# Performance work log

Hardware: AMD Instinct MI355X
Metric: run time of the kernel (lower is better)

The kernel has to match this reference:

```python
import jax, jax.numpy as jnp
import numpy as np
from jax import lax

B, H_IMG, W_IMG, DIM, HEADS = 8, 128, 128, 192, 8
SPLIT = (4, 16)
HB = HEADS // 2            # heads per branch
CB = DIM // 2              # channels per branch
POS_DIM = (CB // 4) // 4   # DynamicPosBias hidden dim = 6


def _make_rel(Hsp, Wsp):
    # rpe_biases table coords and relative_position_index, exactly as in torch buffers
    bh = np.arange(1 - Hsp, Hsp)
    bw = np.arange(1 - Wsp, Wsp)
    biases = np.stack(np.meshgrid(bh, bw, indexing='ij')).reshape(2, -1).T.astype(np.float32)
    coords = np.stack(np.meshgrid(np.arange(Hsp), np.arange(Wsp), indexing='ij')).reshape(2, -1)
    rel = (coords[:, :, None] - coords[:, None, :]).transpose(1, 2, 0).copy()
    rel[:, :, 0] += Hsp - 1
    rel[:, :, 1] += Wsp - 1
    rel[:, :, 0] *= 2 * Wsp - 1
    return jnp.asarray(biases), jnp.asarray(rel.sum(-1))


def _ln(x, g, b):
    m = x.mean(-1, keepdims=True)
    v = ((x - m) ** 2).mean(-1, keepdims=True)
    return (x - m) * lax.rsqrt(v + 1e-5) * g + b


def _dyn_bias(bi, pw, pb, g1, b1, w1, c1, g2, b2, w2, c2, g3, b3, w3, c3):
    # residual=False path: pos3(pos2(pos1(pos_proj(biases)))); posN = Linear(ReLU(LN(.)))
    p = bi @ pw.T + pb
    p = jax.nn.relu(_ln(p, g1, b1)) @ w1.T + c1
    p = jax.nn.relu(_ln(p, g2, b2)) @ w2.T + c2
    return jax.nn.relu(_ln(p, g3, b3)) @ w3.T + c3  # (M, HB)


def _branch(q, k, v, H, W, Hsp, Wsp, rel_idx, biases, pp):
    Bq, L, Cb = q.shape
    N = Hsp * Wsp
    hd = Cb // HB
    def win(t):  # (B, L, Cb) -> (B*nW, HB, N, hd)
        t = t.reshape(Bq, H // Hsp, Hsp, W // Wsp, Wsp, Cb).transpose(0, 1, 3, 2, 4, 5)
        return t.reshape(-1, N, HB, hd).transpose(0, 2, 1, 3)
    qw, kw, vw = win(q), win(k), win(v)
    attn = jnp.einsum('whnd,whmd->whnm', qw * (hd ** -0.5), kw)
    pos = _dyn_bias(biases, *pp)
    rpb = pos[rel_idx.reshape(-1)].reshape(N, N, HB).transpose(2, 0, 1)  # (HB, N, N)
    attn = jax.nn.softmax(attn + rpb[None], axis=-1)
    z = jnp.einsum('whnm,whmd->whnd', attn, vw).transpose(0, 2, 1, 3).reshape(-1, N, Cb)
    z = z.reshape(Bq, H // Hsp, W // Wsp, Hsp, Wsp, Cb).transpose(0, 1, 3, 2, 4, 5)
    return z.reshape(Bq, H * W, Cb)


def _bn(x, g, b, m, v):  # eval-mode BatchNorm2d, NCHW
    sc = (g * lax.rsqrt(v + 1e-5))[None, :, None, None]
    return (x - m[None, :, None, None]) * sc + b[None, :, None, None]


def _fwd(x1, x2, qkv_w, proj_w, proj_b, pw, pb, g1, b1, w1, c1, g2, b2, w2, c2,
         g3, b3, w3, c3, dw_w, dw_b, bn1_g, bn1_b, bn1_m, bn1_v,
         si_w1, si_b1, bn2_g, bn2_b, bn2_m, bn2_v, si_w2, si_b2, H, W):
    Bx, L, C = x1.shape
    qkv1 = (x1 @ qkv_w.T).reshape(Bx, L, 3, C)
    qkv2 = (x2 @ qkv_w.T).reshape(Bx, L, 3, C)
    q1, v1 = qkv1[:, :, 0], qkv1[:, :, 2]
    k2 = qkv2[:, :, 1]
    Ch = C // 2
    bi0, ri0 = _make_rel(SPLIT[0], SPLIT[1])  # idx=0: Hsp, Wsp = split
    bi1, ri1 = _make_rel(SPLIT[1], SPLIT[0])  # idx=1: swapped
    pos_all = (pw, pb, g1, b1, w1, c1, g2, b2, w2, c2, g3, b3, w3, c3)
    pp0 = tuple(a[0] for a in pos_all)
    pp1 = tuple(a[1] for a in pos_all)
    xa = _branch(q1[..., :Ch], k2[..., :Ch], v1[..., :Ch], H, W, SPLIT[0], SPLIT[1], ri0, bi0, pp0)
    xb = _branch(q1[..., Ch:], k2[..., Ch:], v1[..., Ch:], H, W, SPLIT[1], SPLIT[0], ri1, bi1, pp1)
    attened = jnp.concatenate([xa, xb], axis=-1)  # (B, L, C)
    # conv branch: depthwise 3x3 + BN + GELU on v
    v_img = v1.transpose(0, 2, 1).reshape(Bx, C, H, W)
    conv_x = lax.conv_general_dilated(v_img, dw_w, (1, 1), 'SAME',
                                      feature_group_count=C,
                                      dimension_numbers=('NCHW', 'OIHW', 'NCHW'))
    conv_x = conv_x + dw_b[None, :, None, None]
    conv_x = jax.nn.gelu(_bn(conv_x, bn1_g, bn1_b, bn1_m, bn1_v), approximate=False)
    # spatial interaction map from the attention branch (1x1 conv -> BN -> GELU -> 1x1 conv)
    attn_img = attened.transpose(0, 2, 1).reshape(Bx, C, H, W)
    s = jnp.einsum('oc,bchw->bohw', si_w1, attn_img) + si_b1[None, :, None, None]
    s = jax.nn.gelu(_bn(s, bn2_g, bn2_b, bn2_m, bn2_v), approximate=False)
    s = jnp.einsum('oc,bchw->bohw', si_w2, s) + si_b2[None, :, None, None]  # (B,1,H,W)
    conv_x = jax.nn.sigmoid(s) * conv_x
    conv_x = conv_x.transpose(0, 2, 3, 1).reshape(Bx, L, C)
    return (attened + conv_x) @ proj_w.T + proj_b


def setup_inputs() -> dict:
    key = jax.random.key(0)
    ks = jax.random.split(key, 16)
    L = H_IMG * W_IMG
    def n(k, shape, s=0.05):
        return jax.random.normal(k, shape, jnp.float32) * s
    d = {}
    d['x1'] = jax.random.normal(ks[0], (B, L, DIM), jnp.float32)
    d['x2'] = jax.random.normal(ks[1], (B, L, DIM), jnp.float32)
    d['qkv_w'] = n(ks[2], (3 * DIM, DIM))
    d['proj_w'] = n(ks[3], (DIM, DIM))
    d['proj_b'] = jnp.zeros((DIM,), jnp.float32)
    d['pw'] = n(ks[4], (2, POS_DIM, 2), 0.2)
    d['pb'] = jnp.zeros((2, POS_DIM), jnp.float32)
    d['g1'] = jnp.ones((2, POS_DIM), jnp.float32); d['b1'] = jnp.zeros((2, POS_DIM), jnp.float32)
    d['w1'] = n(ks[5], (2, POS_DIM, POS_DIM), 0.2); d['c1'] = jnp.zeros((2, POS_DIM), jnp.float32)
    d['g2'] = jnp.ones((2, POS_DIM), jnp.float32); d['b2'] = jnp.zeros((2, POS_DIM), jnp.float32)
    d['w2'] = n(ks[6], (2, POS_DIM, POS_DIM), 0.2); d['c2'] = jnp.zeros((2, POS_DIM), jnp.float32)
    d['g3'] = jnp.ones((2, POS_DIM), jnp.float32); d['b3'] = jnp.zeros((2, POS_DIM), jnp.float32)
    d['w3'] = n(ks[7], (2, HB, POS_DIM), 0.2); d['c3'] = jnp.zeros((2, HB), jnp.float32)
    d['dw_w'] = n(ks[8], (DIM, 1, 3, 3), 0.2); d['dw_b'] = jnp.zeros((DIM,), jnp.float32)
    d['bn1_g'] = jnp.ones((DIM,), jnp.float32); d['bn1_b'] = jnp.zeros((DIM,), jnp.float32)
    d['bn1_m'] = n(ks[9], (DIM,), 0.1)
    d['bn1_v'] = jax.random.uniform(ks[10], (DIM,), jnp.float32, 0.5, 1.5)
    d['si_w1'] = n(ks[11], (DIM // 2, DIM)); d['si_b1'] = jnp.zeros((DIM // 2,), jnp.float32)
    d['bn2_g'] = jnp.ones((DIM // 2,), jnp.float32); d['bn2_b'] = jnp.zeros((DIM // 2,), jnp.float32)
    d['bn2_m'] = n(ks[12], (DIM // 2,), 0.1)
    d['bn2_v'] = jax.random.uniform(ks[13], (DIM // 2,), jnp.float32, 0.5, 1.5)
    d['si_w2'] = n(ks[14], (1, DIM // 2), 0.2); d['si_b2'] = jnp.zeros((1,), jnp.float32)
    d['H'] = H_IMG
    d['W'] = W_IMG
    return d


def reference(x1, x2, qkv_w, proj_w, proj_b, pw, pb, g1, b1, w1, c1, g2, b2, w2, c2,
              g3, b3, w3, c3, dw_w, dw_b, bn1_g, bn1_b, bn1_m, bn1_v,
              si_w1, si_b1, bn2_g, bn2_b, bn2_m, bn2_v, si_w2, si_b2, H, W):
    return _fwd(x1, x2, qkv_w, proj_w, proj_b, pw, pb, g1, b1, w1, c1, g2, b2, w2, c2,
                g3, b3, w3, c3, dw_w, dw_b, bn1_g, bn1_b, bn1_m, bn1_v,
                si_w1, si_b1, bn2_g, bn2_b, bn2_m, bn2_v, si_w2, si_b2, int(H), int(W))
```

## Files before the change

### kernel.cpp

```cpp
#include <hip/hip_runtime.h>
#include <hip/hip_bf16.h>
#include <math.h>

#define BDIM 8
#define HH 128
#define WW 128
#define LL (HH*WW)
#define CC 192
#define CBh 96
#define HBn 4
#define HDd 24
#define PD 6
#define RTAB 217

typedef unsigned short ushortT;
typedef __bf16 bf16x8 __attribute__((ext_vector_type(8)));
typedef float f32x4 __attribute__((ext_vector_type(4)));

__device__ __forceinline__ float b2f(ushortT u){
  union { float f; unsigned u; } x; x.u = ((unsigned)u) << 16; return x.f;
}
__device__ __forceinline__ ushortT f2b(float f){
  union { float f; unsigned u; } x; x.f = f;
  unsigned r = x.u + 0x7fffu + ((x.u >> 16) & 1u);
  return (ushortT)(r >> 16);
}
__device__ __forceinline__ float lo16(unsigned u){ union { float f; unsigned u; } x; x.u = u << 16; return x.f; }
__device__ __forceinline__ float hi16(unsigned u){ union { float f; unsigned u; } x; x.u = u & 0xffff0000u; return x.f; }
__device__ __forceinline__ unsigned pack2(float a, float b){
  return (unsigned)f2b(a) | ((unsigned)f2b(b) << 16);
}
__device__ __forceinline__ void unpack8(uint4 u, float* f){
  f[0]=lo16(u.x); f[1]=hi16(u.x); f[2]=lo16(u.y); f[3]=hi16(u.y);
  f[4]=lo16(u.z); f[5]=hi16(u.z); f[6]=lo16(u.w); f[7]=hi16(u.w);
}
__device__ __forceinline__ unsigned cvt2(float a, float b){
  __hip_bfloat162 h = __float22bfloat162_rn(float2{a, b});
  union { __hip_bfloat162 h; unsigned u; } c; c.h = h; return c.u;
}
__device__ __forceinline__ float gelu_exact(float x){
  return 0.5f * x * (1.0f + erff(x * 0.70710678118654752f));
}

union ABu { unsigned u[4]; bf16x8 v; };

__device__ __forceinline__ void stage_B512(const ushortT* __restrict__ Wsrc, char* lds){
  int t = threadIdx.x;
  #pragma unroll
  for (int i = 0; i < 9; i++){
    int c = t + i*512;
    int n = c / 24, kc = c - n*24;
    uint4 v = *(const uint4*)(const void*)(Wsrc + n*CC + kc*8);
    int byte = n*384 + kc*16;
    byte ^= ((n & 7) << 4);
    *(uint4*)(lds + byte) = v;
  }
}
__device__ __forceinline__ bf16x8 ldsB(const char* lds, int row, int kbyte){
  int byte = row*384 + kbyte;
  byte ^= ((row & 7) << 4);
  return *(const bf16x8*)(lds + byte);
}

__device__ __forceinline__ void ln_relu6(float* p, const float* g, const float* b){
  float m = 0.f;
  #pragma unroll
  for (int j=0;j<PD;j++) m += p[j];
  m *= (1.0f/PD);
  float v = 0.f;
  #pragma unroll
  for (int j=0;j<PD;j++){ float d = p[j]-m; v += d*d; }
  v *= (1.0f/PD);
  float is = rsqrtf(v + 1e-5f);
  #pragma unroll
  for (int j=0;j<PD;j++){ float t = (p[j]-m)*is*g[j] + b[j]; p[j] = t > 0.f ? t : 0.f; }
}
__device__ __forceinline__ void mm6(float* p, const float* w, const float* c){
  float q[PD];
  #pragma unroll
  for (int j=0;j<PD;j++){
    float a = c[j];
    #pragma unroll
    for (int i=0;i<PD;i++) a += p[i]*w[j*PD+i];
    q[j] = a;
  }
  #pragma unroll
  for (int j=0;j<PD;j++) p[j] = q[j];
}

__global__ void k_pos(const float* __restrict__ pw, const float* __restrict__ pb,
                      const float* __restrict__ g1, const float* __restrict__ b1,
                      const float* __restrict__ w1, const float* __restrict__ c1,
                      const float* __restrict__ g2, const float* __restrict__ b2,
                      const float* __restrict__ w2, const float* __restrict__ c2,
                      const float* __restrict__ g3, const float* __restrict__ b3,
                      const float* __restrict__ w3, const float* __restrict__ c3,
                      float* __restrict__ pos){
  int br = blockIdx.x;
  int r = threadIdx.x;
  if (r >= RTAB) return;
  int Hsp = br ? 16 : 4, Wsp = br ? 4 : 16;
  int W2 = 2*Wsp - 1;
  float bi0 = (float)(r / W2 - (Hsp-1));
  float bi1 = (float)(r % W2 - (Wsp-1));
  const float* PW = pw + br*PD*2;
  const float* PB = pb + br*PD;
  float p[PD];
  #pragma unroll
  for (int j=0;j<PD;j++) p[j] = PW[j*2]*bi0 + PW[j*2+1]*bi1 + PB[j];
  ln_relu6(p, g1+br*PD, b1+br*PD);
  mm6(p, w1+br*PD*PD, c1+br*PD);
  ln_relu6(p, g2+br*PD, b2+br*PD);
  mm6(p, w2+br*PD*PD, c2+br*PD);
  ln_relu6(p, g3+br*PD, b3+br*PD);
  const float* W3 = w3 + br*HBn*PD;
  const float* C3 = c3 + br*HBn;
  #pragma unroll
  for (int h=0;h<HBn;h++){
    float a = C3[h];
    #pragma unroll
    for (int i=0;i<PD;i++) a += p[i]*W3[h*PD+i];
    pos[((size_t)br*RTAB + r)*HBn + h] = a;
  }
}

#define WQKV_ELEMS (3*CC*CC)
#define WPROJ_ELEMS (CC*CC)
#define WSI_ELEMS (CC*CBh)
#define WALL_PAIRS ((WQKV_ELEMS+WPROJ_ELEMS+WSI_ELEMS)/2)

__global__ void k_cvtw(const float* __restrict__ qkv_w, const float* __restrict__ proj_w,
                       const float* __restrict__ si_w1,
                       const float* __restrict__ si_b1,
                       const float* __restrict__ g, const float* __restrict__ bb,
                       const float* __restrict__ mn, const float* __restrict__ vv,
                       const float* __restrict__ si_w2,
                       const float* __restrict__ dw_w, const float* __restrict__ dw_b,
                       const float* __restrict__ bn1_g, const float* __restrict__ bn1_b,
                       const float* __restrict__ bn1_m, const float* __restrict__ bn1_v,
                       ushortT* __restrict__ wb, float* __restrict__ gparam,
                       float* __restrict__ cparam, ushortT* __restrict__ dwt){
  int t = threadIdx.x;
  if (blockIdx.x == 0 && t < CBh){
    float sc = g[t]*rsqrtf(vv[t]+1e-5f);
    gparam[t]        = sc;
    gparam[CBh+t]    = (si_b1[t]-mn[t])*sc + bb[t];
    gparam[2*CBh+t]  = si_w2[t];
  }
  if (blockIdx.x == 1){
    if (t < CC){
      float sc = bn1_g[t]*rsqrtf(bn1_v[t]+1e-5f);
      cparam[t]      = sc;
      cparam[CC+t]   = (dw_b[t]-bn1_m[t])*sc + bn1_b[t];
    }
    for (int i = t; i < 9*CC; i += 256){
      int k = i / CC, c = i - k*CC;
      dwt[i] = f2b(dw_w[c*9 + k]);
    }
  }
  int i = blockIdx.x*256 + t;
  if (i >= WALL_PAIRS) return;
  int e = i*2;
  float a, b;
  if (e < WQKV_ELEMS){ a = qkv_w[e]; b = qkv_w[e+1]; }
  else if (e < WQKV_ELEMS+WPROJ_ELEMS){ a = proj_w[e-WQKV_ELEMS]; b = proj_w[e-WQKV_ELEMS+1]; }
  else { a = si_w1[e-WQKV_ELEMS-WPROJ_ELEMS]; b = si_w1[e-WQKV_ELEMS-WPROJ_ELEMS+1]; }
  *(unsigned*)(void*)(wb + e) = cvt2(a, b);
}

__global__ __launch_bounds__(512, 4) void k_qkv(const float* __restrict__ x1, const float* __restrict__ x2,
                                                const ushortT* __restrict__ wb,
                                                ushortT* __restrict__ q1, ushortT* __restrict__ k2,
                                                ushortT* __restrict__ v1){
  __shared__ char Bs[CC*CC*2];
  int z = blockIdx.y;
  const float* src = (z == 1) ? x2 : x1;
  ushortT* dst = (z == 0) ? q1 : ((z == 1) ? k2 : v1);
  stage_B512(wb + (size_t)z*CC*CC, Bs);

  int w = threadIdx.x >> 6, l = threadIdx.x & 63;
  int row0 = blockIdx.x*128 + w*16;
  int lr = l & 15;
  int hk = l >> 4;
  f32x4 acc[12];
  #pragma unroll
  for (int n=0; n<12; n++) acc[n] = (f32x4){0.f,0.f,0.f,0.f};

  const float* ap = src + (size_t)(row0 + lr)*CC + hk*8;
  __syncthreads();

  #pragma unroll
  for (int ks = 0; ks < 6; ks++){
    float4 p0 = *(const float4*)(ap + ks*32);
    float4 p1 = *(const float4*)(ap + ks*32 + 4);
    ABu a;
    a.u[0] = cvt2(p0.x, p0.y); a.u[1] = cvt2(p0.z, p0.w);
    a.u[2] = cvt2(p1.x, p1.y); a.u[3] = cvt2(p1.z, p1.w);
    int kb = ks*64 + hk*16;
    #pragma unroll
    for (int n=0; n<12; n++){
      bf16x8 bfr = ldsB(Bs, n*16 + lr, kb);
      acc[n] = __builtin_amdgcn_mfma_f32_16x16x32_bf16(a.v, bfr, acc[n], 0, 0, 0);
    }
  }
  int crow = hk*4, ccol = lr;
  #pragma unroll
  for (int n=0; n<12; n++)
    #pragma unroll
    for (int r=0; r<4; r++){
      int m = row0 + crow + r;
      dst[(size_t)m*CC + n*16 + ccol] = f2b(acc[n][r]);
    }
}

template<int HSP, int WSP>
__global__ __launch_bounds__(256) void k_attn(const ushortT* __restrict__ q1, const ushortT* __restrict__ k2,
                                              const ushortT* __restrict__ v1, const float* __restrict__ pos,
                                              ushortT* __restrict__ att){
  constexpr int BR = (HSP == 4) ? 0 : 1;
  constexpr int NWH = HH / HSP, NWW = WW / WSP;
  constexpr int CH0 = BR * CBh;
  __shared__ float ks[64][CBh];
  __shared__ float vs[64][CBh];
  __shared__ float ps[RTAB*HBn];
  int t = threadIdx.x;
  int wid = blockIdx.x;
  int b = wid / (NWH*NWW);
  int rem = wid - b*(NWH*NWW);
  int hi = rem / NWW, wj = rem - hi*NWW;
  for (int i = t; i < RTAB*HBn; i += 256) ps[i] = pos[(size_t)BR*RTAB*HBn + i];
  #pragma unroll
  for (int r = 0; r < 3; r++){
    int idx = t + r*256;
    int pix = idx / 12, seg = idx - pix*12;
    int ii = pix / WSP, jj = pix - ii*WSP;
    size_t base = (((size_t)b*LL) + (size_t)(hi*HSP+ii)*WW + wj*WSP + jj)*CC + CH0 + seg*8;
    uint4 uk = *(const uint4*)(const void*)(k2 + base);
    unpack8(uk, &ks[pix][seg*8]);
    uint4 uv = *(const uint4*)(const void*)(v1 + base);
    unpack8(uv, &vs[pix][seg*8]);
  }
  __syncthreads();
  int h = t >> 6, lane = t & 63;
  int i1 = lane / WSP, j1 = lane - i1*WSP;
  size_t lq = ((size_t)b*LL) + (size_t)(hi*HSP+i1)*WW + wj*WSP + j1;
  const ushortT* qrow = q1 + lq*CC + CH0 + h*HDd;
  float qf[HDd];
  #pragma unroll
  for (int d0 = 0; d0 < HDd; d0 += 8){
    uint4 u = *(const uint4*)(const void*)(qrow + d0);
    unpack8(u, &qf[d0]);
  }
  #pragma unroll
  for (int d=0; d<HDd; d++) qf[d] *= 0.20412414523193154f;
  float lg[64];
  #pragma unroll
  for (int m = 0; m < 64; m++){
    const float* kr = &ks[m][h*HDd];
    float s = 0.f;
    #pragma unroll
    for (int d=0; d<HDd; d++) s = fmaf(qf[d], kr[d], s);
    int i2 = m / WSP, j2 = m - i2*WSP;
    int ridx = (i1-i2+HSP-1)*(2*WSP-1) + (j1-j2+WSP-1);
    lg[m] = s + ps[ridx*HBn + h];
  }
  float mx = lg[0];
  #pragma unroll
  for (int m=1;m<64;m++) mx = fmaxf(mx, lg[m]);
  float sum = 0.f;
  #pragma unroll
  for (int m=0;m<64;m++){ lg[m] = __expf(lg[m]-mx); sum += lg[m]; }
  float inv = 1.0f / sum;
  float z[HDd];
  #pragma unroll
  for (int d=0;d<HDd;d++) z[d] = 0.f;
  #pragma unroll
  for (int m=0;m<64;m++){
    float p = lg[m]*inv;
    const float* vr = &vs[m][h*HDd];
    #pragma unroll
    for (int d=0;d<HDd;d++) z[d] = fmaf(p, vr[d], z[d]);
  }
  ushortT* orow = att + lq*CC + CH0 + h*HDd;
  #pragma unroll
  for (int d0=0; d0<HDd; d0+=8){
    uint4 u;
    u.x = pack2(z[d0+0], z[d0+1]);
    u.y = pack2(z[d0+2], z[d0+3]);
    u.z = pack2(z[d0+4], z[d0+5]);
    u.w = pack2(z[d0+6], z[d0+7]);
    *(uint4*)(void*)(orow + d0) = u;
  }
}

__global__ __launch_bounds__(256) void k_conv(const ushortT* __restrict__ v1,
                                              const ushortT* __restrict__ dwt,
                                              const float* __restrict__ cparam,
                                              ushortT* __restrict__ cx){
  int tid = blockIdx.x*256 + threadIdx.x;
  int grp = tid % 24;
  int pix = tid / 24;
  int j = pix & (WW-1);
  int rest = pix >> 7;
  int i = rest & (HH-1);
  int b = rest >> 7;
  int c0 = grp*8;
  uint4 wreg[9];
  #pragma unroll
  for (int k=0;k<9;k++) wreg[k] = *(const uint4*)(const void*)(dwt + k*CC + c0);
  float acc[8];
  #pragma unroll
  for (int t2=0;t2<8;t2++) acc[t2]=0.f;
  #pragma unroll
  for (int ki=0;ki<3;ki++){
    int ii = i + ki - 1;
    if (ii < 0 || ii >= HH) continue;
    #pragma unroll
    for (int kj=0;kj<3;kj++){
      int jj = j + kj - 1;
      if (jj < 0 || jj >= WW) continue;
      uint4 uv = *(const uint4*)(const void*)(v1 + (((size_t)b*LL) + (size_t)ii*WW + jj)*CC + c0);
      float fv[8], fw[8];
      unpack8(uv, fv);
      unpack8(wreg[ki*3+kj], fw);
      #pragma unroll
      for (int t2=0;t2<8;t2++) acc[t2] = fmaf(fv[t2], fw[t2], acc[t2]);
    }
  }
  float4 s0 = *(const float4*)(cparam + c0);
  float4 s1 = *(const float4*)(cparam + c0 + 4);
  float4 o0 = *(const float4*)(cparam + CC + c0);
  float4 o1 = *(const float4*)(cparam + CC + c0 + 4);
  float scv[8] = {s0.x,s0.y,s0.z,s0.w,s1.x,s1.y,s1.z,s1.w};
  float ofv[8] = {o0.x,o0.y,o0.z,o0.w,o1.x,o1.y,o1.z,o1.w};
  unsigned ou[4];
  #pragma unroll
  for (int t2=0;t2<4;t2++){
    float y0 = gelu_exact(acc[2*t2]  *scv[2*t2]   + ofv[2*t2]);
    float y1 = gelu_exact(acc[2*t2+1]*scv[2*t2+1] + ofv[2*t2+1]);
    ou[t2] = pack2(y0, y1);
  }
  uint4 res; res.x=ou[0]; res.y=ou[1]; res.z=ou[2]; res.w=ou[3];
  *(uint4*)(void*)(cx + (size_t)pix*CC + c0) = res;
}

__global__ __launch_bounds__(256) void k_gate(const ushortT* __restrict__ att,
                                              const ushortT* __restrict__ wsi,
                                              const float* __restrict__ gparam,
                                              const float* __restrict__ si_b2,
                                              float* __restrict__ gate){
  int w = threadIdx.x >> 6, l = threadIdx.x & 63;
  int row0 = blockIdx.x*128 + w*32;
  int lr = l & 15;
  int lk = (l >> 4) * 8;
  f32x4 acc[2][6];
  #pragma unroll
  for (int rt=0; rt<2; rt++)
    #pragma unroll
    for (int n=0; n<6; n++) acc[rt][n] = (f32x4){0.f,0.f,0.f,0.f};
  #pragma unroll
  for (int ks = 0; ks < 6; ks++){
    int k0 = ks*32 + lk;
    bf16x8 a0 = *(const bf16x8*)(const void*)(att + (size_t)(row0 + lr)*CC + k0);
    bf16x8 a1 = *(const bf16x8*)(const void*)(att + (size_t)(row0 + 16 + lr)*CC + k0);
    #pragma unroll
    for (int n=0; n<6; n++){
      bf16x8 bfr = *(const bf16x8*)(const void*)(wsi + (size_t)(n*16 + lr)*CC + k0);
      acc[0][n] = __builtin_amdgcn_mfma_f32_16x16x32_bf16(a0, bfr, acc[0][n], 0, 0, 0);
      acc[1][n] = __builtin_amdgcn_mfma_f32_16x16x32_bf16(a1, bfr, acc[1][n], 0, 0, 0);
    }
  }
  int crow = (l >> 4) * 4, ccol = l & 15;
  float sc6[6], cb6[6], w26[6];
  #pragma unroll
  for (int n=0; n<6; n++){
    int o = n*16 + ccol;
    sc6[n] = gparam[o];
    cb6[n] = gparam[CBh + o];
    w26[n] = gparam[2*CBh + o];
  }
  float sb2 = si_b2[0];
  float ps[2][4];
  #pragma unroll
  for (int rt=0; rt<2; rt++)
    #pragma unroll
    for (int r=0; r<4; r++) ps[rt][r] = 0.f;
  #pragma unroll
  for (int rt=0; rt<2; rt++)
    #pragma unroll
    for (int n=0; n<6; n++)
      #pragma unroll
      for (int r=0; r<4; r++){
        float x = acc[rt][n][r]*sc6[n] + cb6[n];
        ps[rt][r] += gelu_exact(x) * w26[n];
      }
  #pragma unroll
  for (int rt=0; rt<2; rt++)
    #pragma unroll
    for (int r=0; r<4; r++){
      float v = ps[rt][r];
      #pragma unroll
      for (int off = 1; off < 16; off <<= 1) v += __shfl_xor(v, off, 64);
      ps[rt][r] = v;
    }
  if (ccol == 0){
    #pragma unroll
    for (int rt=0; rt<2; rt++)
      #pragma unroll
      for (int r=0; r<4; r++){
        int m = row0 + rt*16 + crow + r;
        gate[m] = 1.0f / (1.0f + __expf(-(ps[rt][r] + sb2)));
      }
  }
}

__global__ __launch_bounds__(512, 4) void k_proj(const ushortT* __restrict__ att, const ushortT* __restrict__ cx,
                                                 const float* __restrict__ gate,
                                                 const ushortT* __restrict__ wp, const float* __restrict__ pbias,
                                                 float* __restrict__ out){
  __shared__ char Bs[CC*CC*2];
  stage_B512(wp, Bs);

  int w = threadIdx.x >> 6, l = threadIdx.x & 63;
  int row0 = blockIdx.x*128 + w*16;
  int lr = l & 15;
  int hk = l >> 4;
  float gv = gate[row0 + lr];
  f32x4 acc[12];
  #pragma unroll
  for (int n=0; n<12; n++) acc[n] = (f32x4){0.f,0.f,0.f,0.f};

  size_t base = (size_t)(row0 + lr)*CC + hk*8;
  __syncthreads();

  #pragma unroll
  for (int ks = 0; ks < 6; ks++){
    uint4 ua = *(const uint4*)(const void*)(att + base + ks*32);
    uint4 uc = *(const uint4*)(const void*)(cx  + base + ks*32);
    float fa[8], fc[8];
    unpack8(ua, fa); unpack8(uc, fc);
    #pragma unroll
    for (int j=0;j<8;j++) fa[j] = fmaf(gv, fc[j], fa[j]);
    ABu a;
    a.u[0] = cvt2(fa[0], fa[1]); a.u[1] = cvt2(fa[2], fa[3]);
    a.u[2] = cvt2(fa[4], fa[5]); a.u[3] = cvt2(fa[6], fa[7]);
    int kb = ks*64 + hk*16;
    #pragma unroll
    for (int n=0; n<12; n++){
      bf16x8 bfr = ldsB(Bs, n*16 + lr, kb);
      acc[n] = __builtin_amdgcn_mfma_f32_16x16x32_bf16(a.v, bfr, acc[n], 0, 0, 0);
    }
  }
  int crow = hk*4, ccol = lr;
  #pragma unroll
  for (int n=0; n<12; n++){
    float bv = pbias[n*16 + ccol];
    #pragma unroll
    for (int r=0; r<4; r++){
      int m = row0 + crow + r;
      out[(size_t)m*CC + n*16 + ccol] = acc[n][r] + bv;
    }
  }
}

extern "C" void kernel_launch(void* const* d_in, const int* in_sizes, int n_in,
                              void* d_out, int out_size, void* d_ws, size_t ws_size,
                              hipStream_t stream){
  const float* x1    = (const float*)d_in[0];
  const float* x2    = (const float*)d_in[1];
  const float* qkv_w = (const float*)d_in[2];
  const float* proj_w= (const float*)d_in[3];
  const float* proj_b= (const float*)d_in[4];
  const float* pw    = (const float*)d_in[5];
  const float* pb    = (const float*)d_in[6];
  const float* g1    = (const float*)d_in[7];
  const float* b1    = (const float*)d_in[8];
  const float* w1    = (const float*)d_in[9];
  const float* c1    = (const float*)d_in[10];
  const float* g2    = (const float*)d_in[11];
  const float* b2    = (const float*)d_in[12];
  const float* w2    = (const float*)d_in[13];
  const float* c2    = (const float*)d_in[14];
  const float* g3    = (const float*)d_in[15];
  const float* b3    = (const float*)d_in[16];
  const float* w3    = (const float*)d_in[17];
  const float* c3    = (const float*)d_in[18];
  const float* dw_w  = (const float*)d_in[19];
  const float* dw_b  = (const float*)d_in[20];
  const float* bn1_g = (const float*)d_in[21];
  const float* bn1_b = (const float*)d_in[22];
  const float* bn1_m = (const float*)d_in[23];
  const float* bn1_v = (const float*)d_in[24];
  const float* si_w1 = (const float*)d_in[25];
  const float* si_b1 = (const float*)d_in[26];
  const float* bn2_g = (const float*)d_in[27];
  const float* bn2_b = (const float*)d_in[28];
  const float* bn2_m = (const float*)d_in[29];
  const float* bn2_v = (const float*)d_in[30];
  const float* si_w2 = (const float*)d_in[31];
  const float* si_b2 = (const float*)d_in[32];
  float* out = (float*)d_out;

  char* ws = (char*)d_ws;
  const size_t SZ  = (size_t)BDIM * LL * CC;
  const size_t SZB = SZ * 2;
  ushortT* q1   = (ushortT*)(ws);
  ushortT* v1   = (ushortT*)(ws + SZB);
  ushortT* k2   = (ushortT*)(ws + 2*SZB);
  ushortT* att  = (ushortT*)(ws + 3*SZB);
  float*   gate = (float*)  (ws + 4*SZB);
  float*   pos  = (float*)  (ws + 4*SZB + (size_t)BDIM*LL*sizeof(float));
  ushortT* wbf  = (ushortT*)(ws + 4*SZB + (size_t)BDIM*LL*sizeof(float) + 16384);
  ushortT* wproj = wbf + WQKV_ELEMS;
  ushortT* wsi   = wproj + WPROJ_ELEMS;
  float*   gparam = (float*)(wbf + WQKV_ELEMS + WPROJ_ELEMS + WSI_ELEMS);
  float*   cparam = gparam + 3*CBh;
  ushortT* dwt    = (ushortT*)(cparam + 2*CC);
  ushortT* convx = q1;

  k_pos<<<dim3(2), dim3(256), 0, stream>>>(pw,pb,g1,b1,w1,c1,g2,b2,w2,c2,g3,b3,w3,c3,pos);
  k_cvtw<<<dim3((WALL_PAIRS+255)/256), dim3(256), 0, stream>>>(qkv_w, proj_w, si_w1,
      si_b1, bn2_g, bn2_b, bn2_m, bn2_v, si_w2,
      dw_w, dw_b, bn1_g, bn1_b, bn1_m, bn1_v, wbf, gparam, cparam, dwt);
  k_qkv<<<dim3(1024,3), dim3(512), 0, stream>>>(x1, x2, wbf, q1, k2, v1);
  k_attn<4,16><<<dim3(2048), dim3(256), 0, stream>>>(q1, k2, v1, pos, att);
  k_attn<16,4><<<dim3(2048), dim3(256), 0, stream>>>(q1, k2, v1, pos, att);
  k_conv<<<dim3((unsigned)(SZ/8/256)), dim3(256), 0, stream>>>(v1, dwt, cparam, convx);
  k_gate<<<dim3(1024), dim3(256), 0, stream>>>(att, wsi, gparam, si_b2, gate);
  k_proj<<<dim3(1024), dim3(512), 0, stream>>>(att, convx, gate, wproj, proj_b, out);
}
```

Measured before the change: 389.5 us.

## Rewrite window attention kernel to use bf16 MFMA for QK^T and PV

Measured after the change: 325.2 us. 1.2x faster.

```diff
diff --git a/kernel.cpp b/kernel.cpp
--- a/kernel.cpp
+++ b/kernel.cpp
@@ -214,83 +214,142 @@
 }
 
 template<int HSP, int WSP>
-__global__ __launch_bounds__(256) void k_attn(const ushortT* __restrict__ q1, const ushortT* __restrict__ k2,
-                                              const ushortT* __restrict__ v1, const float* __restrict__ pos,
-                                              ushortT* __restrict__ att){
+__global__ __launch_bounds__(256, 2) void k_attn(const ushortT* __restrict__ q1, const ushortT* __restrict__ k2,
+                                                 const ushortT* __restrict__ v1, const float* __restrict__ pos,
+                                                 ushortT* __restrict__ att){
   constexpr int BR = (HSP == 4) ? 0 : 1;
   constexpr int NWH = HH / HSP, NWW = WW / WSP;
   constexpr int CH0 = BR * CBh;
-  __shared__ float ks[64][CBh];
-  __shared__ float vs[64][CBh];
+  constexpr float SCALE = 0.20412414523193154f;
+  __shared__ ushortT poolA[20480];
+  __shared__ ushortT VTs[9216];
   __shared__ float ps[RTAB*HBn];
   int t = threadIdx.x;
   int wid = blockIdx.x;
   int b = wid / (NWH*NWW);
   int rem = wid - b*(NWH*NWW);
-  int hi = rem / NWW, wj = rem - hi*NWW;
+  int wr = rem / NWW, wc = rem - wr*NWW;
+
   for (int i = t; i < RTAB*HBn; i += 256) ps[i] = pos[(size_t)BR*RTAB*HBn + i];
-  #pragma unroll
-  for (int r = 0; r < 3; r++){
-    int idx = t + r*256;
-    int pix = idx / 12, seg = idx - pix*12;
-    int ii = pix / WSP, jj = pix - ii*WSP;
-    size_t base = (((size_t)b*LL) + (size_t)(hi*HSP+ii)*WW + wj*WSP + jj)*CC + CH0 + seg*8;
-    uint4 uk = *(const uint4*)(const void*)(k2 + base);
-    unpack8(uk, &ks[pix][seg*8]);
-    uint4 uv = *(const uint4*)(const void*)(v1 + base);
-    unpack8(uv, &vs[pix][seg*8]);
+
+  #pragma unroll
+  for (int it = 0; it < 3; it++){
+    int e = t + it*256;
+    int p = e / 12, seg = e - p*12;
+    int h = seg / 3, c0 = (seg - h*3)*8;
+    int ii = p / WSP, jj = p - ii*WSP;
+    size_t g = ((size_t)b*LL + (size_t)(wr*HSP + ii)*WW + wc*WSP + jj)*CC + CH0 + h*24 + c0;
+    uint4 uq = *(const uint4*)(const void*)(q1 + g);
+    uint4 uk = *(const uint4*)(const void*)(k2 + g);
+    uint4 uv = *(const uint4*)(const void*)(v1 + g);
+    *(uint4*)(void*)&poolA[(h*64 + p)*40 + c0] = uq;
+    *(uint4*)(void*)&poolA[10240 + (h*64 + p)*40 + c0] = uk;
+    union { uint4 u; ushortT s[8]; } vu; vu.u = uv;
+    #pragma unroll
+    for (int j = 0; j < 8; j++)
+      VTs[(h*32 + c0 + j)*72 + p] = vu.s[j];
+  }
+  {
+    int h = t >> 6, p = t & 63;
+    uint4 z4; z4.x = z4.y = z4.z = z4.w = 0u;
+    *(uint4*)(void*)&poolA[(h*64 + p)*40 + 24] = z4;
+    *(uint4*)(void*)&poolA[10240 + (h*64 + p)*40 + 24] = z4;
   }
   __syncthreads();
-  int h = t >> 6, lane = t & 63;
-  int i1 = lane / WSP, j1 = lane - i1*WSP;
-  size_t lq = ((size_t)b*LL) + (size_t)(hi*HSP+i1)*WW + wj*WSP + j1;
-  const ushortT* qrow = q1 + lq*CC + CH0 + h*HDd;
-  float qf[HDd];
-  #pragma unroll
-  for (int d0 = 0; d0 < HDd; d0 += 8){
-    uint4 u = *(const uint4*)(const void*)(qrow + d0);
-    unpack8(u, &qf[d0]);
-  }
-  #pragma unroll
-  for (int d=0; d<HDd; d++) qf[d] *= 0.20412414523193154f;
-  float lg[64];
-  #pragma unroll
-  for (int m = 0; m < 64; m++){
-    const float* kr = &ks[m][h*HDd];
-    float s = 0.f;
-    #pragma unroll
-    for (int d=0; d<HDd; d++) s = fmaf(qf[d], kr[d], s);
-    int i2 = m / WSP, j2 = m - i2*WSP;
-    int ridx = (i1-i2+HSP-1)*(2*WSP-1) + (j1-j2+WSP-1);
-    lg[m] = s + ps[ridx*HBn + h];
-  }
-  float mx = lg[0];
-  #pragma unroll
-  for (int m=1;m<64;m++) mx = fmaxf(mx, lg[m]);
-  float sum = 0.f;
-  #pragma unroll
-  for (int m=0;m<64;m++){ lg[m] = __expf(lg[m]-mx); sum += lg[m]; }
-  float inv = 1.0f / sum;
-  float z[HDd];
-  #pragma unroll
-  for (int d=0;d<HDd;d++) z[d] = 0.f;
-  #pragma unroll
-  for (int m=0;m<64;m++){
-    float p = lg[m]*inv;
-    const float* vr = &vs[m][h*HDd];
-    #pragma unroll
-    for (int d=0;d<HDd;d++) z[d] = fmaf(p, vr[d], z[d]);
-  }
-  ushortT* orow = att + lq*CC + CH0 + h*HDd;
-  #pragma unroll
-  for (int d0=0; d0<HDd; d0+=8){
-    uint4 u;
-    u.x = pack2(z[d0+0], z[d0+1]);
-    u.y = pack2(z[d0+2], z[d0+3]);
-    u.z = pack2(z[d0+4], z[d0+5]);
-    u.w = pack2(z[d0+6], z[d0+7]);
-    *(uint4*)(void*)(orow + d0) = u;
-  }
+
+  int w = t >> 6, l = t & 63;
+  int lo = l & 15, hi = l >> 4;
+
+  bf16x8 qa[4], kb[4];
+  #pragma unroll
+  for (int mt = 0; mt < 4; mt++)
+    qa[mt] = *(const bf16x8*)(const void*)&poolA[(w*64 + mt*16 + lo)*40 + hi*8];
+  #pragma unroll
+  for (int nt = 0; nt < 4; nt++)
+    kb[nt] = *(const bf16x8*)(const void*)&poolA[10240 + (w*64 + nt*16 + lo)*40 + hi*8];
+  __syncthreads();
+
+  f32x4 sacc[4][4];
+  #pragma unroll
+  for (int mt = 0; mt < 4; mt++)
+    #pragma unroll
+    for (int nt = 0; nt < 4; nt++) sacc[mt][nt] = (f32x4){0.f,0.f,0.f,0.f};
+  #pragma unroll
+  for (int mt = 0; mt < 4; mt++)
+    #pragma unroll
+    for (int nt = 0; nt < 4; nt++)
+      sacc[mt][nt] = __builtin_amdgcn_mfma_f32_16x16x32_bf16(qa[mt], kb[nt], sacc[mt][nt], 0, 0, 0);
+
+  float invl[4][4];
+  #pragma unroll
+  for (int mt = 0; mt < 4; mt++){
+    #pragma unroll
+    for (int r = 0; r < 4; r++){
+      int i = mt*16 + hi*4 + r;
+      int i1 = i / WSP, j1 = i - i1*WSP;
+      float sv[4];
+      #pragma unroll
+      for (int nt = 0; nt < 4; nt++){
+        int j = nt*16 + lo;
+        int i2 = j / WSP, j2 = j - i2*WSP;
+        int ridx = (i1 - i2 + HSP - 1)*(2*WSP - 1) + (j1 - j2 + WSP - 1);
+        sv[nt] = sacc[mt][nt][r]*SCALE + ps[ridx*HBn + w];
+      }
+      float mx = fmaxf(fmaxf(sv[0], sv[1]), fmaxf(sv[2], sv[3]));
+      #pragma unroll
+      for (int off = 1; off < 16; off <<= 1) mx = fmaxf(mx, __shfl_xor(mx, off, 64));
+      float sum = 0.f;
+      #pragma unroll
+      for (int nt = 0; nt < 4; nt++){ sv[nt] = __expf(sv[nt] - mx); sum += sv[nt]; }
+      #pragma unroll
+      for (int off = 1; off < 16; off <<= 1) sum += __shfl_xor(sum, off, 64);
+      invl[mt][r] = 1.0f / sum;
+      #pragma unroll
+      for (int nt = 0; nt < 4; nt++)
+        poolA[(w*64 + i)*72 + nt*16 + lo] = f2b(sv[nt]);
+    }
+  }
+  __syncthreads();
+
+  bf16x8 pa[4][2], vb[2][2];
+  #pragma unroll
+  for (int mt = 0; mt < 4; mt++)
+    #pragma unroll
+    for (int kt = 0; kt < 2; kt++)
+      pa[mt][kt] = *(const bf16x8*)(const void*)&poolA[(w*64 + mt*16 + lo)*72 + kt*32 + hi*8];
+  #pragma unroll
+  for (int nt2 = 0; nt2 < 2; nt2++)
+    #pragma unroll
+    for (int kt = 0; kt < 2; kt++)
+      vb[nt2][kt] = *(const bf16x8*)(const void*)&VTs[(w*32 + nt2*16 + lo)*72 + kt*32 + hi*8];
+
+  f32x4 oacc[4][2];
+  #pragma unroll
+  for (int mt = 0; mt < 4; mt++)
+    #pragma unroll
+    for (int nt2 = 0; nt2 < 2; nt2++) oacc[mt][nt2] = (f32x4){0.f,0.f,0.f,0.f};
+  #pragma unroll
+  for (int mt = 0; mt < 4; mt++)
+    #pragma unroll
+    for (int nt2 = 0; nt2 < 2; nt2++)
+      #pragma unroll
+      for (int kt = 0; kt < 2; kt++)
+        oacc[mt][nt2] = __builtin_amdgcn_mfma_f32_16x16x32_bf16(pa[mt][kt], vb[nt2][kt], oacc[mt][nt2], 0, 0, 0);
+
+  #pragma unroll
+  for (int mt = 0; mt < 4; mt++)
+    #pragma unroll
+    for (int nt2 = 0; nt2 < 2; nt2++){
+      int d = nt2*16 + lo;
+      if (nt2 == 1 && lo >= 8) continue;
+      #pragma unroll
+      for (int r = 0; r < 4; r++){
+        int i = mt*16 + hi*4 + r;
+        int ii = i / WSP, jj = i - ii*WSP;
+        size_t g = ((size_t)b*LL + (size_t)(wr*HSP + ii)*WW + wc*WSP + jj)*CC + CH0 + w*24 + d;
+        att[g] = f2b(oacc[mt][nt2][r] * invl[mt][r]);
+      }
+    }
 }
 
 __global__ __launch_bounds__(256) void k_conv(const ushortT* __restrict__ v1,
```
